# Optimization experiments

Hardware: AMD Instinct MI355X
Metric: run time of the kernel (lower is better)

The kernel has to match this reference:

```python
import jax, jax.numpy as jnp
import numpy as np

# Filter defaults from the torch module
SCORE_THR = 0.05
IOU_THR = 0.5
MAX_DET = 300
K_PRE = 512          # candidate pool for fixed-size NMS (>= MAX_DET)
BBOX_STD = jnp.array([0.1, 0.1, 0.2, 0.2], dtype=jnp.float32)  # retinanet-style bbox_transform_inv std
IMG = 800.0


def setup_inputs() -> dict:
    key = jax.random.key(0)
    k1, k2, k3, k4 = jax.random.split(key, 4)
    B, N, C = 8, 200000, 80
    # valid xyxy anchors: centers in [0, 800], sizes in [16, 256]
    ctr = jax.random.uniform(k1, (B, N, 2), dtype=jnp.float32) * IMG
    wh = 16.0 + jax.random.uniform(k2, (B, N, 2), dtype=jnp.float32) * 240.0
    anchors = jnp.concatenate([ctr - 0.5 * wh, ctr + 0.5 * wh], axis=-1)
    reg = jax.random.normal(k3, (B, N, 4), dtype=jnp.float32)
    cls = jax.random.uniform(k4, (B, N, C), dtype=jnp.float32)
    sizes = jnp.full((B, 2), IMG, dtype=jnp.float32)  # (h, w) per image
    return {"anchors": anchors, "reg": reg, "cls": cls, "sizes": sizes}


def bbox_transform_inv(anchors, reg):
    # anchors, reg: [B, N, 4] xyxy / deltas
    w = anchors[..., 2] - anchors[..., 0]
    h = anchors[..., 3] - anchors[..., 1]
    cx = anchors[..., 0] + 0.5 * w
    cy = anchors[..., 1] + 0.5 * h
    dx, dy, dw, dh = (reg * BBOX_STD)[..., 0], (reg * BBOX_STD)[..., 1], (reg * BBOX_STD)[..., 2], (reg * BBOX_STD)[..., 3]
    pcx = cx + dx * w
    pcy = cy + dy * h
    pw = jnp.exp(dw) * w
    ph = jnp.exp(dh) * h
    return jnp.stack([pcx - 0.5 * pw, pcy - 0.5 * ph, pcx + 0.5 * pw, pcy + 0.5 * ph], axis=-1)


def clip_boxes(bbox, sizes):
    # ClipBoxes: x coords clipped to [0, w=sizes[:,1]], y coords to [0, h=sizes[:,0]]
    w = sizes[:, 1][:, None]
    h = sizes[:, 0][:, None]
    x1 = jnp.clip(bbox[..., 0], 0.0, w)
    y1 = jnp.clip(bbox[..., 1], 0.0, h)
    x2 = jnp.clip(bbox[..., 2], 0.0, w)
    y2 = jnp.clip(bbox[..., 3], 0.0, h)
    return jnp.stack([x1, y1, x2, y2], axis=-1)


def pairwise_iou(b):
    # b: [K, 4] -> [K, K]
    area = (b[:, 2] - b[:, 0]) * (b[:, 3] - b[:, 1])
    lt = jnp.maximum(b[:, None, :2], b[None, :, :2])
    rb = jnp.minimum(b[:, None, 2:], b[None, :, 2:])
    wh = jnp.clip(rb - lt, 0.0)
    inter = wh[..., 0] * wh[..., 1]
    return inter / (area[:, None] + area[None, :] - inter + 1e-9)


def greedy_nms_keep(boxes, valid):
    # boxes: [K, 4] already sorted by descending score; valid: [K] bool
    K = boxes.shape[0]
    iou = pairwise_iou(boxes)
    idx = jnp.arange(K)
    def body(i, keep):
        sup = (iou[i] > IOU_THR) & (idx > i) & keep[i]
        return keep & ~sup
    keep = jax.lax.fori_loop(0, K, body, valid)
    return keep


def filter_one(boxes, scores, labels):
    # boxes [N,4], scores [N], labels [N] -> padded (MAX_DET) outputs, pad = -1
    masked = jnp.where(scores > SCORE_THR, scores, -jnp.inf)
    top_s, top_i = jax.lax.top_k(masked, K_PRE)          # sorted descending
    cand_b = boxes[top_i]                                 # [K_PRE, 4]
    cand_l = labels[top_i]
    cand_valid = top_s > SCORE_THR
    keep = greedy_nms_keep(cand_b, cand_valid)
    kept_s = jnp.where(keep, top_s, -jnp.inf)
    det_s, det_i = jax.lax.top_k(kept_s, MAX_DET)
    det_b = cand_b[det_i]
    det_l = cand_l[det_i]
    ok = det_s > -jnp.inf
    out_b = jnp.where(ok[:, None], det_b, -1.0)
    out_s = jnp.where(ok, det_s, -1.0)[:, None]
    out_l = jnp.where(ok, det_l.astype(jnp.float32), -1.0)[:, None]
    return out_b, out_s, out_l


def reference(anchors, reg, cls, sizes):
    bbox = bbox_transform_inv(anchors, reg)   # [B, N, 4]
    bbox = clip_boxes(bbox, sizes)
    scores = jnp.max(cls, axis=-1)            # class_specific_filter=False path
    labels = jnp.argmax(cls, axis=-1)
    select_boxes, select_scores, select_labels = jax.vmap(filter_one)(bbox, scores, labels)
    return select_boxes, select_scores, select_labels
```

## Files before the change

kernel.cpp:

```cpp
#include <hip/hip_runtime.h>
#include <hip/hip_bf16.h>
#include <math.h>

#define KPRE 512
#define CAP 4096
#define MAXDET 300
#define SCORE_THR 0.05f
#define IOU_THR 0.5f
#define NREP 16
#define NSEL 32

__device__ __forceinline__ unsigned key_bin(unsigned key) {
    return (key >> 10) & 0xFFFFu;
}

template<int F4A>
__global__ __launch_bounds__(256)
void score_label_kernel(const float* __restrict__ cls,
                        unsigned* __restrict__ keys,
                        unsigned char* __restrict__ labels,
                        int N) {
    const int b = blockIdx.y;
    const int tid = threadIdx.x;
    const int g = tid >> 2, q = tid & 3;
    const int a = blockIdx.x * 64 + g;
    if (a >= N) return;
    const float4* p = (const float4*)cls + ((size_t)b * N + a) * F4A;

    float4 vv[F4A / 4];
#pragma unroll
    for (int j = 0; j < F4A / 4; ++j) vv[j] = p[q + 4 * j];

    unsigned long long best = 0ull;
#pragma unroll
    for (int j = 0; j < F4A / 4; ++j) {
        float4 v = vv[j];
        int cbase = (q + 4 * j) * 4;
        float m = v.x; int c = cbase;
        if (v.y > m) { m = v.y; c = cbase + 1; }
        if (v.z > m) { m = v.z; c = cbase + 2; }
        if (v.w > m) { m = v.w; c = cbase + 3; }
        unsigned long long comp =
            ((unsigned long long)__float_as_uint(m) << 32) | (unsigned)(255 - c);
        if (comp > best) best = comp;
    }
    unsigned long long o;
    o = (unsigned long long)__shfl_xor((long long)best, 1, 64); if (o > best) best = o;
    o = (unsigned long long)__shfl_xor((long long)best, 2, 64); if (o > best) best = o;

    if (q == 0) {
        unsigned sb = (unsigned)(best >> 32);
        unsigned cl = 255u - (unsigned)(best & 0xFFFFFFFFull);
        size_t idx = (size_t)b * N + a;
        keys[idx] = (__uint_as_float(sb) > SCORE_THR) ? sb : 0u;
        labels[idx] = (unsigned char)cl;
    }
}

__global__ __launch_bounds__(256)
void score_label_generic(const float* __restrict__ cls,
                         unsigned* __restrict__ keys,
                         unsigned char* __restrict__ labels,
                         int N, int C) {
    const int b = blockIdx.y;
    const int tid = threadIdx.x;
    const int g = tid >> 2, q = tid & 3;
    const int a = blockIdx.x * 64 + g;
    if (a >= N) return;
    const int F4A = C >> 2;
    const float4* p = (const float4*)cls + ((size_t)b * N + a) * F4A;
    unsigned long long best = 0ull;
    for (int f4 = q; f4 < F4A; f4 += 4) {
        float4 v = p[f4];
        int cbase = f4 * 4;
        float m = v.x; int c = cbase;
        if (v.y > m) { m = v.y; c = cbase + 1; }
        if (v.z > m) { m = v.z; c = cbase + 2; }
        if (v.w > m) { m = v.w; c = cbase + 3; }
        unsigned long long comp =
            ((unsigned long long)__float_as_uint(m) << 32) | (unsigned)(255 - c);
        if (comp > best) best = comp;
    }
    unsigned long long o;
    o = (unsigned long long)__shfl_xor((long long)best, 1, 64); if (o > best) best = o;
    o = (unsigned long long)__shfl_xor((long long)best, 2, 64); if (o > best) best = o;
    if (q == 0) {
        unsigned sb = (unsigned)(best >> 32);
        unsigned cl = 255u - (unsigned)(best & 0xFFFFFFFFull);
        size_t idx = (size_t)b * N + a;
        keys[idx] = (__uint_as_float(sb) > SCORE_THR) ? sb : 0u;
        labels[idx] = (unsigned char)cl;
    }
}

__global__ __launch_bounds__(256)
void init_kernel(unsigned* __restrict__ ghist1, unsigned* __restrict__ ghist2,
                 int* __restrict__ gmeta, unsigned* __restrict__ gH,
                 unsigned* __restrict__ gcnt, int B) {
    const int t = blockIdx.x * 256 + threadIdx.x;
    if (t < B * 256) { ghist1[t] = 0u; ghist2[t] = 0u; }
    if (t < B) { gmeta[2 * t] = -1; gmeta[2 * t + 1] = 0; gH[t] = 1u; gcnt[t] = 0u; }
}

__global__ __launch_bounds__(256)
void hist_coarse_kernel(const unsigned* __restrict__ keys,
                        unsigned* __restrict__ ghist1, int N) {
    const int b = blockIdx.y, tid = threadIdx.x;
    __shared__ unsigned h[NREP * 256];
    for (int i = tid; i < NREP * 256; i += 256) h[i] = 0u;
    __syncthreads();
    const unsigned rrep = (tid & (NREP - 1)) * 256;
    const unsigned* kb = keys + (size_t)b * N;
    const uint4* k4 = (const uint4*)kb;
    const int N4 = N >> 2;
    for (int i = blockIdx.x * 256 + tid; i < N4; i += 256 * NSEL) {
        uint4 v = k4[i];
        if (v.x) atomicAdd(&h[rrep + (key_bin(v.x) >> 8)], 1u);
        if (v.y) atomicAdd(&h[rrep + (key_bin(v.y) >> 8)], 1u);
        if (v.z) atomicAdd(&h[rrep + (key_bin(v.z) >> 8)], 1u);
        if (v.w) atomicAdd(&h[rrep + (key_bin(v.w) >> 8)], 1u);
    }
    if (blockIdx.x == 0) {
        for (int i = (N4 << 2) + tid; i < N; i += 256) {
            unsigned kk = kb[i];
            if (kk) atomicAdd(&h[rrep + (key_bin(kk) >> 8)], 1u);
        }
    }
    __syncthreads();
    unsigned s = 0;
    for (int j = 0; j < NREP; ++j) s += h[j * 256 + tid];
    if (s) atomicAdd(&ghist1[b * 256 + tid], s);
}

__global__ __launch_bounds__(256)
void thresh1_kernel(const unsigned* __restrict__ ghist1, int* __restrict__ gmeta) {
    const int b = blockIdx.x, tid = threadIdx.x;
    __shared__ unsigned sscan[256];
    sscan[tid] = ghist1[b * 256 + tid];
    __syncthreads();
    for (int off = 1; off < 256; off <<= 1) {
        unsigned v = sscan[tid] + ((tid + off < 256) ? sscan[tid + off] : 0u);
        __syncthreads();
        sscan[tid] = v;
        __syncthreads();
    }
    unsigned above = (tid < 255) ? sscan[tid + 1] : 0u;
    if (sscan[tid] >= KPRE && above < KPRE) {
        gmeta[2 * b] = tid;
        gmeta[2 * b + 1] = (int)above;
    }
}

__global__ __launch_bounds__(256)
void hist_fine_kernel(const unsigned* __restrict__ keys,
                      const int* __restrict__ gmeta,
                      unsigned* __restrict__ ghist2, int N) {
    const int b = blockIdx.y, tid = threadIdx.x;
    const int h1 = gmeta[2 * b];
    if (h1 < 0) return;
    __shared__ unsigned h[NREP * 256];
    for (int i = tid; i < NREP * 256; i += 256) h[i] = 0u;
    __syncthreads();
    const unsigned rrep = (tid & (NREP - 1)) * 256;
    const unsigned* kb = keys + (size_t)b * N;
    const uint4* k4 = (const uint4*)kb;
    const int N4 = N >> 2;
    for (int i = blockIdx.x * 256 + tid; i < N4; i += 256 * NSEL) {
        uint4 v = k4[i];
        unsigned fb;
        if (v.x) { fb = key_bin(v.x); if ((int)(fb >> 8) == h1) atomicAdd(&h[rrep + (fb & 255u)], 1u); }
        if (v.y) { fb = key_bin(v.y); if ((int)(fb >> 8) == h1) atomicAdd(&h[rrep + (fb & 255u)], 1u); }
        if (v.z) { fb = key_bin(v.z); if ((int)(fb >> 8) == h1) atomicAdd(&h[rrep + (fb & 255u)], 1u); }
        if (v.w) { fb = key_bin(v.w); if ((int)(fb >> 8) == h1) atomicAdd(&h[rrep + (fb & 255u)], 1u); }
    }
    if (blockIdx.x == 0) {
        for (int i = (N4 << 2) + tid; i < N; i += 256) {
            unsigned kk = kb[i];
            if (kk) { unsigned fb = key_bin(kk); if ((int)(fb >> 8) == h1) atomicAdd(&h[rrep + (fb & 255u)], 1u); }
        }
    }
    __syncthreads();
    unsigned s = 0;
    for (int j = 0; j < NREP; ++j) s += h[j * 256 + tid];
    if (s) atomicAdd(&ghist2[b * 256 + tid], s);
}

__global__ __launch_bounds__(256)
void thresh2_kernel(const unsigned* __restrict__ ghist2,
                    const int* __restrict__ gmeta, unsigned* __restrict__ gH) {
    const int b = blockIdx.x, tid = threadIdx.x;
    const int h1 = gmeta[2 * b];
    if (h1 < 0) return;
    const unsigned above = (unsigned)gmeta[2 * b + 1];
    __shared__ unsigned sscan[256];
    sscan[tid] = ghist2[b * 256 + tid];
    __syncthreads();
    for (int off = 1; off < 256; off <<= 1) {
        unsigned v = sscan[tid] + ((tid + off < 256) ? sscan[tid + off] : 0u);
        __syncthreads();
        sscan[tid] = v;
        __syncthreads();
    }
    unsigned abv = ((tid < 255) ? sscan[tid + 1] : 0u) + above;
    if (sscan[tid] + above >= KPRE && abv < KPRE) {
        unsigned H = ((unsigned)h1 << 8) + (unsigned)tid;
        gH[b] = H ? H : 1u;
    }
}

__device__ __forceinline__ void emit_cand(unsigned key, unsigned idx, unsigned H,
                                          unsigned long long* __restrict__ cand,
                                          unsigned* __restrict__ cnt, int lane) {
    bool m = key_bin(key) >= H;
    unsigned long long mk = __ballot(m);
    if (!mk) return;
    int leader = __ffsll(mk) - 1;
    unsigned basep = 0;
    if (lane == leader) basep = atomicAdd(cnt, (unsigned)__popcll(mk));
    basep = (unsigned)__shfl((int)basep, leader, 64);
    if (m) {
        unsigned p = basep + (unsigned)__popcll(mk & ((1ull << lane) - 1ull));
        if (p < CAP) cand[p] = ((unsigned long long)key << 32) | ~idx;
    }
}

__global__ __launch_bounds__(256)
void collect_kernel(const unsigned* __restrict__ keys,
                    const unsigned* __restrict__ gH,
                    unsigned long long* __restrict__ gcand,
                    unsigned* __restrict__ gcnt, int N) {
    const int b = blockIdx.y, tid = threadIdx.x;
    const int lane = tid & 63;
    const unsigned H = gH[b];
    const unsigned* kb = keys + (size_t)b * N;
    const uint4* k4 = (const uint4*)kb;
    const int N4 = N >> 2;
    unsigned long long* cand = gcand + (size_t)b * CAP;
    unsigned* cnt = gcnt + b;
    for (int i = blockIdx.x * 256 + tid; i < N4; i += 256 * NSEL) {
        uint4 v = k4[i];
        unsigned base = (unsigned)(i << 2);
        emit_cand(v.x, base, H, cand, cnt, lane);
        emit_cand(v.y, base + 1u, H, cand, cnt, lane);
        emit_cand(v.z, base + 2u, H, cand, cnt, lane);
        emit_cand(v.w, base + 3u, H, cand, cnt, lane);
    }
    if (blockIdx.x == 0) {
        for (int i = (N4 << 2) + tid; i < N; i += 256)
            emit_cand(kb[i], (unsigned)i, H, cand, cnt, lane);
    }
}

__global__ __launch_bounds__(1024, 1)
void final_nms_kernel(const float* __restrict__ anchors,
                      const float* __restrict__ reg,
                      const float* __restrict__ sizes,
                      const unsigned char* __restrict__ labels,
                      const unsigned long long* __restrict__ gcand,
                      const unsigned* __restrict__ gcnt,
                      float* __restrict__ out,
                      int N, int B) {
    const int b = blockIdx.x;
    const int tid = threadIdx.x;
    const int nthr = blockDim.x;

    __shared__ __align__(16) unsigned long long buf[CAP];
    unsigned* sup = (unsigned*)buf;
    __shared__ float4 boxs[KPRE];
    __shared__ float areas[KPRE];
    __shared__ unsigned ckey[KPRE];
    __shared__ unsigned cidx[KPRE];
    __shared__ unsigned validw[16], keepw_s[16], wpref[17];
    __shared__ int sh_M;

    int cnt = (int)gcnt[b];
    if (cnt > CAP) cnt = CAP;
    const unsigned long long* cand = gcand + (size_t)b * CAP;
    for (int i = tid; i < cnt; i += nthr) buf[i] = cand[i];
    if (tid == 0) {
        int M = KPRE;
        while (M < cnt) M <<= 1;
        sh_M = M;
    }
    __syncthreads();
    const int M = sh_M;
    for (int i2 = cnt + tid; i2 < M; i2 += nthr) buf[i2] = 0ull;
    __syncthreads();

    for (int kk = 2; kk <= M; kk <<= 1) {
        for (int j = kk >> 1; j > 0; j >>= 1) {
            for (int i2 = tid; i2 < M; i2 += nthr) {
                int l = i2 ^ j;
                if (l > i2) {
                    unsigned long long a = buf[i2], c = buf[l];
                    bool desc = ((i2 & kk) == 0);
                    if (desc ? (a < c) : (a > c)) { buf[i2] = c; buf[l] = a; }
                }
            }
            __syncthreads();
        }
    }

    const float wimg = sizes[b * 2 + 1];
    const float himg = sizes[b * 2 + 0];
    for (int t = tid; t < KPRE; t += nthr) {
        unsigned long long c = buf[t];
        unsigned key = (unsigned)(c >> 32);
        unsigned ai = ~(unsigned)(c & 0xFFFFFFFFull);
        bool valid = (key != 0u) && (t < cnt);
        ckey[t] = valid ? key : 0u;
        cidx[t] = valid ? ai : 0u;
        float4 bx = make_float4(0.f, 0.f, 0.f, 0.f);
        if (valid) {
            const float4 a4 = *(const float4*)(anchors + ((size_t)b * N + ai) * 4);
            const float4 r4 = *(const float4*)(reg + ((size_t)b * N + ai) * 4);
            float w = a4.z - a4.x, h = a4.w - a4.y;
            float cx = a4.x + 0.5f * w, cy = a4.y + 0.5f * h;
            float dx = r4.x * 0.1f, dy = r4.y * 0.1f;
            float dw = r4.z * 0.2f, dh = r4.w * 0.2f;
            float pcx = cx + dx * w, pcy = cy + dy * h;
            float pw = expf(dw) * w, ph = expf(dh) * h;
            float x1 = pcx - 0.5f * pw, y1 = pcy - 0.5f * ph;
            float x2 = pcx + 0.5f * pw, y2 = pcy + 0.5f * ph;
            bx.x = fminf(fmaxf(x1, 0.f), wimg);
            bx.y = fminf(fmaxf(y1, 0.f), himg);
            bx.z = fminf(fmaxf(x2, 0.f), wimg);
            bx.w = fminf(fmaxf(y2, 0.f), himg);
        }
        boxs[t] = bx;
        areas[t] = (bx.z - bx.x) * (bx.w - bx.y);
    }
    __syncthreads();

    for (int unit = tid; unit < KPRE * 16; unit += nthr) {
        int i = unit >> 4, w = unit & 15;
        float4 bi = boxs[i];
        float ai = areas[i];
        unsigned bits = 0;
        int j0 = w * 32;
        for (int bit = 0; bit < 32; ++bit) {
            int j = j0 + bit;
            if (j > i) {
                float4 bj = boxs[j];
                float ltx = fmaxf(bi.x, bj.x), lty = fmaxf(bi.y, bj.y);
                float rbx = fminf(bi.z, bj.z), rby = fminf(bi.w, bj.w);
                float iw = fmaxf(rbx - ltx, 0.f), ih = fmaxf(rby - lty, 0.f);
                float inter = iw * ih;
                float iou = inter / (ai + areas[j] - inter + 1e-9f);
                if (iou > IOU_THR) bits |= (1u << bit);
            }
        }
        sup[i * 16 + w] = bits;
    }
    __syncthreads();

    unsigned long long bal = __ballot(tid < KPRE && ckey[tid] != 0u);
    if (tid < KPRE && (tid & 63) == 0) {
        validw[(tid >> 6) * 2] = (unsigned)(bal & 0xFFFFFFFFull);
        validw[(tid >> 6) * 2 + 1] = (unsigned)(bal >> 32);
    }
    __syncthreads();

    if (tid < 64) {
        unsigned kw = (tid < 16) ? validw[tid] : 0u;
        for (int i = 0; i < KPRE; ++i) {
            unsigned rw = sup[i * 16 + (tid & 15)];
            unsigned ow = __shfl(kw, i >> 5, 64);
            if ((ow >> (i & 31)) & 1u) kw &= ~rw;
        }
        if (tid < 16) keepw_s[tid] = kw;
    }
    __syncthreads();

    if (tid == 0) {
        unsigned s = 0;
        for (int w2 = 0; w2 < 16; ++w2) { wpref[w2] = s; s += __popc(keepw_s[w2]); }
        wpref[16] = s;
    }
    __syncthreads();
    const unsigned nk = wpref[16];

    float* ob = out;
    float* os = out + (size_t)B * MAXDET * 4;
    float* ol = os + (size_t)B * MAXDET;
    const unsigned char* lb = labels + (size_t)b * N;

    for (int t = tid; t < KPRE; t += nthr) {
        unsigned word = keepw_s[t >> 5];
        if ((word >> (t & 31)) & 1u) {
            unsigned rank = wpref[t >> 5] + __popc(word & ((1u << (t & 31)) - 1u));
            if (rank < MAXDET) {
                float4 bx = boxs[t];
                size_t ro = (size_t)b * MAXDET + rank;
                ob[ro * 4 + 0] = bx.x;
                ob[ro * 4 + 1] = bx.y;
                ob[ro * 4 + 2] = bx.z;
                ob[ro * 4 + 3] = bx.w;
                os[ro] = __uint_as_float(ckey[t]);
                ol[ro] = (float)lb[cidx[t]];
            }
        }
    }
    for (int r = tid; r < MAXDET; r += nthr) {
        if (r >= (int)nk) {
            size_t ro = (size_t)b * MAXDET + r;
            ob[ro * 4 + 0] = -1.f;
            ob[ro * 4 + 1] = -1.f;
            ob[ro * 4 + 2] = -1.f;
            ob[ro * 4 + 3] = -1.f;
            os[ro] = -1.f;
            ol[ro] = -1.f;
        }
    }
}

extern "C" void kernel_launch(void* const* d_in, const int* in_sizes, int n_in,
                              void* d_out, int out_size, void* d_ws, size_t ws_size,
                              hipStream_t stream) {
    const float* anchors = (const float*)d_in[0];
    const float* reg     = (const float*)d_in[1];
    const float* cls     = (const float*)d_in[2];
    const float* sizes   = (const float*)d_in[3];

    const int B = in_sizes[3] / 2;
    const int N = in_sizes[0] / (4 * B);
    const int C = in_sizes[2] / (B * N);
    const int total = B * N;

    char* ws = (char*)d_ws;
    size_t off = 0;
    unsigned* keys = (unsigned*)(ws + off);            off += (size_t)total * 4;
    unsigned char* labels = (unsigned char*)(ws + off); off += (size_t)total;
    off = (off + 255) & ~(size_t)255;
    unsigned* ghist1 = (unsigned*)(ws + off);          off += (size_t)B * 256 * 4;
    unsigned* ghist2 = (unsigned*)(ws + off);          off += (size_t)B * 256 * 4;
    int* gmeta = (int*)(ws + off);                     off += (size_t)B * 2 * 4;
    unsigned* gH = (unsigned*)(ws + off);              off += (size_t)B * 4;
    unsigned* gcnt = (unsigned*)(ws + off);            off += (size_t)B * 4;
    off = (off + 255) & ~(size_t)255;
    unsigned long long* gcand = (unsigned long long*)(ws + off);

    float* out = (float*)d_out;

    dim3 blkA(256);
    dim3 grdA((N + 63) / 64, B);
    if (C == 80)
        score_label_kernel<20><<<grdA, blkA, 0, stream>>>(cls, keys, labels, N);
    else
        score_label_generic<<<grdA, blkA, 0, stream>>>(cls, keys, labels, N, C);

    init_kernel<<<dim3((B * 256 + 255) / 256), dim3(256), 0, stream>>>(ghist1, ghist2, gmeta, gH, gcnt, B);
    hist_coarse_kernel<<<dim3(NSEL, B), dim3(256), 0, stream>>>(keys, ghist1, N);
    thresh1_kernel<<<dim3(B), dim3(256), 0, stream>>>(ghist1, gmeta);
    hist_fine_kernel<<<dim3(NSEL, B), dim3(256), 0, stream>>>(keys, gmeta, ghist2, N);
    thresh2_kernel<<<dim3(B), dim3(256), 0, stream>>>(ghist2, gmeta, gH);
    collect_kernel<<<dim3(NSEL, B), dim3(256), 0, stream>>>(keys, gH, gcand, gcnt, N);
    final_nms_kernel<<<dim3(B), dim3(1024), 0, stream>>>(anchors, reg, sizes, labels, gcand, gcnt, out, N, B);
}
```

Before: 908.5 us.

## Fuse coarse histogram into score pass and fold threshold scans into consumers

The coarse radix histogram is now built inside the score/label kernel, using a shared-memory histogram per block that is flushed into one of four replicated global histograms. This removes a full pass over the keys. The two threshold kernels are gone: each block of the fine-histogram and collect kernels redoes the 256-bin scans itself. The NMS IoU loop also skips the lower-triangle words instead of testing j>i for every bit. The cost is 256 extra global atomics per score block, which could contend, plus redundant scans in every block.

```diff
diff --git a/kernel.cpp b/kernel.cpp
--- a/kernel.cpp
+++ b/kernel.cpp
@@ -8,10 +8,20 @@
 #define SCORE_THR 0.05f
 #define IOU_THR 0.5f
 #define NREP 16
+#define NGR 4
 #define NSEL 32
 
 __device__ __forceinline__ unsigned key_bin(unsigned key) {
     return (key >> 10) & 0xFFFFu;
+}
+
+__global__ __launch_bounds__(256)
+void init_kernel(unsigned* __restrict__ ghist1, unsigned* __restrict__ ghist2,
+                 unsigned* __restrict__ gcnt, int B) {
+    const int t = blockIdx.x * 256 + threadIdx.x;
+    if (t < B * NGR * 256) ghist1[t] = 0u;
+    if (t < B * 256) ghist2[t] = 0u;
+    if (t < B) gcnt[t] = 0u;
 }
 
 template<int F4A>
@@ -19,124 +29,117 @@
 void score_label_kernel(const float* __restrict__ cls,
                         unsigned* __restrict__ keys,
                         unsigned char* __restrict__ labels,
+                        unsigned* __restrict__ ghist1,
                         int N) {
     const int b = blockIdx.y;
     const int tid = threadIdx.x;
     const int g = tid >> 2, q = tid & 3;
     const int a = blockIdx.x * 64 + g;
-    if (a >= N) return;
-    const float4* p = (const float4*)cls + ((size_t)b * N + a) * F4A;
-
-    float4 vv[F4A / 4];
+
+    __shared__ unsigned lh[4 * 256];
+    for (int i = tid; i < 4 * 256; i += 256) lh[i] = 0u;
+    __syncthreads();
+
+    const bool active = (a < N);
+    if (active) {
+        const float4* p = (const float4*)cls + ((size_t)b * N + a) * F4A;
+
+        float4 vv[F4A / 4];
 #pragma unroll
-    for (int j = 0; j < F4A / 4; ++j) vv[j] = p[q + 4 * j];
-
-    unsigned long long best = 0ull;
+        for (int j = 0; j < F4A / 4; ++j) vv[j] = p[q + 4 * j];
+
+        unsigned long long best = 0ull;
 #pragma unroll
-    for (int j = 0; j < F4A / 4; ++j) {
-        float4 v = vv[j];
-        int cbase = (q + 4 * j) * 4;
-        float m = v.x; int c = cbase;
-        if (v.y > m) { m = v.y; c = cbase + 1; }
-        if (v.z > m) { m = v.z; c = cbase + 2; }
-        if (v.w > m) { m = v.w; c = cbase + 3; }
-        unsigned long long comp =
-            ((unsigned long long)__float_as_uint(m) << 32) | (unsigned)(255 - c);
-        if (comp > best) best = comp;
-    }
-    unsigned long long o;
-    o = (unsigned long long)__shfl_xor((long long)best, 1, 64); if (o > best) best = o;
-    o = (unsigned long long)__shfl_xor((long long)best, 2, 64); if (o > best) best = o;
-
-    if (q == 0) {
-        unsigned sb = (unsigned)(best >> 32);
-        unsigned cl = 255u - (unsigned)(best & 0xFFFFFFFFull);
-        size_t idx = (size_t)b * N + a;
-        keys[idx] = (__uint_as_float(sb) > SCORE_THR) ? sb : 0u;
-        labels[idx] = (unsigned char)cl;
-    }
+        for (int j = 0; j < F4A / 4; ++j) {
+            float4 v = vv[j];
+            int cbase = (q + 4 * j) * 4;
+            float m = v.x; int c = cbase;
+            if (v.y > m) { m = v.y; c = cbase + 1; }
+            if (v.z > m) { m = v.z; c = cbase + 2; }
+            if (v.w > m) { m = v.w; c = cbase + 3; }
+            unsigned long long comp =
+                ((unsigned long long)__float_as_uint(m) << 32) | (unsigned)(255 - c);
+            if (comp > best) best = comp;
+        }
+        unsigned long long o;
+        o = (unsigned long long)__shfl_xor((long long)best, 1, 64); if (o > best) best = o;
+        o = (unsigned long long)__shfl_xor((long long)best, 2, 64); if (o > best) best = o;
+
+        if (q == 0) {
+            unsigned sb = (unsigned)(best >> 32);
+            unsigned cl = 255u - (unsigned)(best & 0xFFFFFFFFull);
+            size_t idx = (size_t)b * N + a;
+            unsigned keyv = (__uint_as_float(sb) > SCORE_THR) ? sb : 0u;
+            keys[idx] = keyv;
+            labels[idx] = (unsigned char)cl;
+            if (keyv) atomicAdd(&lh[(g & 3) * 256 + (key_bin(keyv) >> 8)], 1u);
+        }
+    }
+    __syncthreads();
+    unsigned s = lh[tid] + lh[256 + tid] + lh[512 + tid] + lh[768 + tid];
+    if (s) atomicAdd(&ghist1[((size_t)b * NGR + (blockIdx.x & (NGR - 1))) * 256 + tid], s);
 }
 
 __global__ __launch_bounds__(256)
 void score_label_generic(const float* __restrict__ cls,
                          unsigned* __restrict__ keys,
                          unsigned char* __restrict__ labels,
+                         unsigned* __restrict__ ghist1,
                          int N, int C) {
     const int b = blockIdx.y;
     const int tid = threadIdx.x;
     const int g = tid >> 2, q = tid & 3;
     const int a = blockIdx.x * 64 + g;
-    if (a >= N) return;
-    const int F4A = C >> 2;
-    const float4* p = (const float4*)cls + ((size_t)b * N + a) * F4A;
-    unsigned long long best = 0ull;
-    for (int f4 = q; f4 < F4A; f4 += 4) {
-        float4 v = p[f4];
-        int cbase = f4 * 4;
-        float m = v.x; int c = cbase;
-        if (v.y > m) { m = v.y; c = cbase + 1; }
-        if (v.z > m) { m = v.z; c = cbase + 2; }
-        if (v.w > m) { m = v.w; c = cbase + 3; }
-        unsigned long long comp =
-            ((unsigned long long)__float_as_uint(m) << 32) | (unsigned)(255 - c);
-        if (comp > best) best = comp;
-    }
-    unsigned long long o;
-    o = (unsigned long long)__shfl_xor((long long)best, 1, 64); if (o > best) best = o;
-    o = (unsigned long long)__shfl_xor((long long)best, 2, 64); if (o > best) best = o;
-    if (q == 0) {
-        unsigned sb = (unsigned)(best >> 32);
-        unsigned cl = 255u - (unsigned)(best & 0xFFFFFFFFull);
-        size_t idx = (size_t)b * N + a;
-        keys[idx] = (__uint_as_float(sb) > SCORE_THR) ? sb : 0u;
-        labels[idx] = (unsigned char)cl;
-    }
+
+    __shared__ unsigned lh[4 * 256];
+    for (int i = tid; i < 4 * 256; i += 256) lh[i] = 0u;
+    __syncthreads();
+
+    const bool active = (a < N);
+    if (active) {
+        const int F4A = C >> 2;
+        const float4* p = (const float4*)cls + ((size_t)b * N + a) * F4A;
+        unsigned long long best = 0ull;
+        for (int f4 = q; f4 < F4A; f4 += 4) {
+            float4 v = p[f4];
+            int cbase = f4 * 4;
+            float m = v.x; int c = cbase;
+            if (v.y > m) { m = v.y; c = cbase + 1; }
+            if (v.z > m) { m = v.z; c = cbase + 2; }
+            if (v.w > m) { m = v.w; c = cbase + 3; }
+            unsigned long long comp =
+                ((unsigned long long)__float_as_uint(m) << 32) | (unsigned)(255 - c);
+            if (comp > best) best = comp;
+        }
+        unsigned long long o;
+        o = (unsigned long long)__shfl_xor((long long)best, 1, 64); if (o > best) best = o;
+        o = (unsigned long long)__shfl_xor((long long)best, 2, 64); if (o > best) best = o;
+        if (q == 0) {
+            unsigned sb = (unsigned)(best >> 32);
+            unsigned cl = 255u - (unsigned)(best & 0xFFFFFFFFull);
+            size_t idx = (size_t)b * N + a;
+            unsigned keyv = (__uint_as_float(sb) > SCORE_THR) ? sb : 0u;
+            keys[idx] = keyv;
+            labels[idx] = (unsigned char)cl;
+            if (keyv) atomicAdd(&lh[(g & 3) * 256 + (key_bin(keyv) >> 8)], 1u);
+        }
+    }
+    __syncthreads();
+    unsigned s = lh[tid] + lh[256 + tid] + lh[512 + tid] + lh[768 + tid];
+    if (s) atomicAdd(&ghist1[((size_t)b * NGR + (blockIdx.x & (NGR - 1))) * 256 + tid], s);
 }
 
 __global__ __launch_bounds__(256)
-void init_kernel(unsigned* __restrict__ ghist1, unsigned* __restrict__ ghist2,
-                 int* __restrict__ gmeta, unsigned* __restrict__ gH,
-                 unsigned* __restrict__ gcnt, int B) {
-    const int t = blockIdx.x * 256 + threadIdx.x;
-    if (t < B * 256) { ghist1[t] = 0u; ghist2[t] = 0u; }
-    if (t < B) { gmeta[2 * t] = -1; gmeta[2 * t + 1] = 0; gH[t] = 1u; gcnt[t] = 0u; }
-}
-
-__global__ __launch_bounds__(256)
-void hist_coarse_kernel(const unsigned* __restrict__ keys,
-                        unsigned* __restrict__ ghist1, int N) {
+void hist_fine_kernel(const unsigned* __restrict__ keys,
+                      const unsigned* __restrict__ ghist1,
+                      unsigned* __restrict__ ghist2, int N) {
     const int b = blockIdx.y, tid = threadIdx.x;
-    __shared__ unsigned h[NREP * 256];
-    for (int i = tid; i < NREP * 256; i += 256) h[i] = 0u;
-    __syncthreads();
-    const unsigned rrep = (tid & (NREP - 1)) * 256;
-    const unsigned* kb = keys + (size_t)b * N;
-    const uint4* k4 = (const uint4*)kb;
-    const int N4 = N >> 2;
-    for (int i = blockIdx.x * 256 + tid; i < N4; i += 256 * NSEL) {
-        uint4 v = k4[i];
-        if (v.x) atomicAdd(&h[rrep + (key_bin(v.x) >> 8)], 1u);
-        if (v.y) atomicAdd(&h[rrep + (key_bin(v.y) >> 8)], 1u);
-        if (v.z) atomicAdd(&h[rrep + (key_bin(v.z) >> 8)], 1u);
-        if (v.w) atomicAdd(&h[rrep + (key_bin(v.w) >> 8)], 1u);
-    }
-    if (blockIdx.x == 0) {
-        for (int i = (N4 << 2) + tid; i < N; i += 256) {
-            unsigned kk = kb[i];
-            if (kk) atomicAdd(&h[rrep + (key_bin(kk) >> 8)], 1u);
-        }
-    }
-    __syncthreads();
-    unsigned s = 0;
-    for (int j = 0; j < NREP; ++j) s += h[j * 256 + tid];
-    if (s) atomicAdd(&ghist1[b * 256 + tid], s);
-}
-
-__global__ __launch_bounds__(256)
-void thresh1_kernel(const unsigned* __restrict__ ghist1, int* __restrict__ gmeta) {
-    const int b = blockIdx.x, tid = threadIdx.x;
     __shared__ unsigned sscan[256];
-    sscan[tid] = ghist1[b * 256 + tid];
+    __shared__ int sh_h1;
+    __shared__ unsigned lh[NREP * 256];
+    if (tid == 0) sh_h1 = -1;
+    const unsigned* g1 = ghist1 + (size_t)b * NGR * 256;
+    sscan[tid] = g1[tid] + g1[256 + tid] + g1[512 + tid] + g1[768 + tid];
     __syncthreads();
     for (int off = 1; off < 256; off <<= 1) {
         unsigned v = sscan[tid] + ((tid + off < 256) ? sscan[tid + off] : 0u);
@@ -144,22 +147,15 @@
         sscan[tid] = v;
         __syncthreads();
     }
-    unsigned above = (tid < 255) ? sscan[tid + 1] : 0u;
-    if (sscan[tid] >= KPRE && above < KPRE) {
-        gmeta[2 * b] = tid;
-        gmeta[2 * b + 1] = (int)above;
-    }
-}
-
-__global__ __launch_bounds__(256)
-void hist_fine_kernel(const unsigned* __restrict__ keys,
-                      const int* __restrict__ gmeta,
-                      unsigned* __restrict__ ghist2, int N) {
-    const int b = blockIdx.y, tid = threadIdx.x;
-    const int h1 = gmeta[2 * b];
+    {
+        unsigned above = (tid < 255) ? sscan[tid + 1] : 0u;
+        if (sscan[tid] >= KPRE && above < KPRE) sh_h1 = tid;
+    }
+    __syncthreads();
+    const int h1 = sh_h1;
     if (h1 < 0) return;
-    __shared__ unsigned h[NREP * 256];
-    for (int i = tid; i < NREP * 256; i += 256) h[i] = 0u;
+
+    for (int i = tid; i < NREP * 256; i += 256) lh[i] = 0u;
     __syncthreads();
     const unsigned rrep = (tid & (NREP - 1)) * 256;
     const unsigned* kb = keys + (size_t)b * N;
@@ -168,44 +164,21 @@
     for (int i = blockIdx.x * 256 + tid; i < N4; i += 256 * NSEL) {
         uint4 v = k4[i];
         unsigned fb;
-        if (v.x) { fb = key_bin(v.x); if ((int)(fb >> 8) == h1) atomicAdd(&h[rrep + (fb & 255u)], 1u); }
-        if (v.y) { fb = key_bin(v.y); if ((int)(fb >> 8) == h1) atomicAdd(&h[rrep + (fb & 255u)], 1u); }
-        if (v.z) { fb = key_bin(v.z); if ((int)(fb >> 8) == h1) atomicAdd(&h[rrep + (fb & 255u)], 1u); }
-        if (v.w) { fb = key_bin(v.w); if ((int)(fb >> 8) == h1) atomicAdd(&h[rrep + (fb & 255u)], 1u); }
+        if (v.x) { fb = key_bin(v.x); if ((int)(fb >> 8) == h1) atomicAdd(&lh[rrep + (fb & 255u)], 1u); }
+        if (v.y) { fb = key_bin(v.y); if ((int)(fb >> 8) == h1) atomicAdd(&lh[rrep + (fb & 255u)], 1u); }
+        if (v.z) { fb = key_bin(v.z); if ((int)(fb >> 8) == h1) atomicAdd(&lh[rrep + (fb & 255u)], 1u); }
+        if (v.w) { fb = key_bin(v.w); if ((int)(fb >> 8) == h1) atomicAdd(&lh[rrep + (fb & 255u)], 1u); }
     }
     if (blockIdx.x == 0) {
         for (int i = (N4 << 2) + tid; i < N; i += 256) {
             unsigned kk = kb[i];
-            if (kk) { unsigned fb = key_bin(kk); if ((int)(fb >> 8) == h1) atomicAdd(&h[rrep + (fb & 255u)], 1u); }
+            if (kk) { unsigned fb = key_bin(kk); if ((int)(fb >> 8) == h1) atomicAdd(&lh[rrep + (fb & 255u)], 1u); }
         }
     }
     __syncthreads();
     unsigned s = 0;
-    for (int j = 0; j < NREP; ++j) s += h[j * 256 + tid];
+    for (int j = 0; j < NREP; ++j) s += lh[j * 256 + tid];
     if (s) atomicAdd(&ghist2[b * 256 + tid], s);
-}
-
-__global__ __launch_bounds__(256)
-void thresh2_kernel(const unsigned* __restrict__ ghist2,
-                    const int* __restrict__ gmeta, unsigned* __restrict__ gH) {
-    const int b = blockIdx.x, tid = threadIdx.x;
-    const int h1 = gmeta[2 * b];
-    if (h1 < 0) return;
-    const unsigned above = (unsigned)gmeta[2 * b + 1];
-    __shared__ unsigned sscan[256];
-    sscan[tid] = ghist2[b * 256 + tid];
-    __syncthreads();
-    for (int off = 1; off < 256; off <<= 1) {
-        unsigned v = sscan[tid] + ((tid + off < 256) ? sscan[tid + off] : 0u);
-        __syncthreads();
-        sscan[tid] = v;
-        __syncthreads();
-    }
-    unsigned abv = ((tid < 255) ? sscan[tid + 1] : 0u) + above;
-    if (sscan[tid] + above >= KPRE && abv < KPRE) {
-        unsigned H = ((unsigned)h1 << 8) + (unsigned)tid;
-        gH[b] = H ? H : 1u;
-    }
 }
 
 __device__ __forceinline__ void emit_cand(unsigned key, unsigned idx, unsigned H,
@@ -226,12 +199,50 @@
 
 __global__ __launch_bounds__(256)
 void collect_kernel(const unsigned* __restrict__ keys,
-                    const unsigned* __restrict__ gH,
+                    const unsigned* __restrict__ ghist1,
+                    const unsigned* __restrict__ ghist2,
                     unsigned long long* __restrict__ gcand,
                     unsigned* __restrict__ gcnt, int N) {
     const int b = blockIdx.y, tid = threadIdx.x;
+    __shared__ unsigned sscan[256];
+    __shared__ int sh_h1;
+    __shared__ unsigned sh_above, sh_H;
+    if (tid == 0) { sh_h1 = -1; sh_H = 1u; }
+    const unsigned* g1 = ghist1 + (size_t)b * NGR * 256;
+    sscan[tid] = g1[tid] + g1[256 + tid] + g1[512 + tid] + g1[768 + tid];
+    __syncthreads();
+    for (int off = 1; off < 256; off <<= 1) {
+        unsigned v = sscan[tid] + ((tid + off < 256) ? sscan[tid + off] : 0u);
+        __syncthreads();
+        sscan[tid] = v;
+        __syncthreads();
+    }
+    {
+        unsigned above = (tid < 255) ? sscan[tid + 1] : 0u;
+        if (sscan[tid] >= KPRE && above < KPRE) { sh_h1 = tid; sh_above = above; }
+    }
+    __syncthreads();
+    const int h1 = sh_h1;
+    unsigned H = 1u;
+    if (h1 >= 0) {
+        sscan[tid] = ghist2[b * 256 + tid];
+        __syncthreads();
+        for (int off = 1; off < 256; off <<= 1) {
+            unsigned v = sscan[tid] + ((tid + off < 256) ? sscan[tid + off] : 0u);
+            __syncthreads();
+            sscan[tid] = v;
+            __syncthreads();
+        }
+        unsigned abv = ((tid < 255) ? sscan[tid + 1] : 0u) + sh_above;
+        if (sscan[tid] + sh_above >= KPRE && abv < KPRE) {
+            unsigned Hc = ((unsigned)h1 << 8) + (unsigned)tid;
+            sh_H = Hc ? Hc : 1u;
+        }
+        __syncthreads();
+        H = sh_H;
+    }
+
     const int lane = tid & 63;
-    const unsigned H = gH[b];
     const unsigned* kb = keys + (size_t)b * N;
     const uint4* k4 = (const uint4*)kb;
     const int N4 = N >> 2;
@@ -334,13 +345,15 @@
 
     for (int unit = tid; unit < KPRE * 16; unit += nthr) {
         int i = unit >> 4, w = unit & 15;
-        float4 bi = boxs[i];
-        float ai = areas[i];
+        int j0 = w * 32;
+        int bstart = i - j0 + 1;
+        if (bstart < 0) bstart = 0;
         unsigned bits = 0;
-        int j0 = w * 32;
-        for (int bit = 0; bit < 32; ++bit) {
-            int j = j0 + bit;
-            if (j > i) {
+        if (bstart < 32) {
+            float4 bi = boxs[i];
+            float ai = areas[i];
+            for (int bit = bstart; bit < 32; ++bit) {
+                int j = j0 + bit;
                 float4 bj = boxs[j];
                 float ltx = fmaxf(bi.x, bj.x), lty = fmaxf(bi.y, bj.y);
                 float rbx = fminf(bi.z, bj.z), rby = fminf(bi.w, bj.w);
@@ -432,28 +445,24 @@
     unsigned* keys = (unsigned*)(ws + off);            off += (size_t)total * 4;
     unsigned char* labels = (unsigned char*)(ws + off); off += (size_t)total;
     off = (off + 255) & ~(size_t)255;
-    unsigned* ghist1 = (unsigned*)(ws + off);          off += (size_t)B * 256 * 4;
+    unsigned* ghist1 = (unsigned*)(ws + off);          off += (size_t)B * NGR * 256 * 4;
     unsigned* ghist2 = (unsigned*)(ws + off);          off += (size_t)B * 256 * 4;
-    int* gmeta = (int*)(ws + off);                     off += (size_t)B * 2 * 4;
-    unsigned* gH = (unsigned*)(ws + off);              off += (size_t)B * 4;
     unsigned* gcnt = (unsigned*)(ws + off);            off += (size_t)B * 4;
     off = (off + 255) & ~(size_t)255;
     unsigned long long* gcand = (unsigned long long*)(ws + off);
 
     float* out = (float*)d_out;
 
+    init_kernel<<<dim3((B * NGR * 256 + 255) / 256), dim3(256), 0, stream>>>(ghist1, ghist2, gcnt, B);
+
     dim3 blkA(256);
     dim3 grdA((N + 63) / 64, B);
     if (C == 80)
-        score_label_kernel<20><<<grdA, blkA, 0, stream>>>(cls, keys, labels, N);
+        score_label_kernel<20><<<grdA, blkA, 0, stream>>>(cls, keys, labels, ghist1, N);
     else
-        score_label_generic<<<grdA, blkA, 0, stream>>>(cls, keys, labels, N, C);
-
-    init_kernel<<<dim3((B * 256 + 255) / 256), dim3(256), 0, stream>>>(ghist1, ghist2, gmeta, gH, gcnt, B);
-    hist_coarse_kernel<<<dim3(NSEL, B), dim3(256), 0, stream>>>(keys, ghist1, N);
-    thresh1_kernel<<<dim3(B), dim3(256), 0, stream>>>(ghist1, gmeta);
-    hist_fine_kernel<<<dim3(NSEL, B), dim3(256), 0, stream>>>(keys, gmeta, ghist2, N);
-    thresh2_kernel<<<dim3(B), dim3(256), 0, stream>>>(ghist2, gmeta, gH);
-    collect_kernel<<<dim3(NSEL, B), dim3(256), 0, stream>>>(keys, gH, gcand, gcnt, N);
+        score_label_generic<<<grdA, blkA, 0, stream>>>(cls, keys, labels, ghist1, N, C);
+
+    hist_fine_kernel<<<dim3(NSEL, B), dim3(256), 0, stream>>>(keys, ghist1, ghist2, N);
+    collect_kernel<<<dim3(NSEL, B), dim3(256), 0, stream>>>(keys, ghist1, ghist2, gcand, gcnt, N);
     final_nms_kernel<<<dim3(B), dim3(1024), 0, stream>>>(anchors, reg, sizes, labels, gcand, gcnt, out, N, B);
 }
```

Result: no change. 907.8 us (-0.1%).
